# Performance work log

Measured on AMD Instinct MI355X. Metric: run time of the kernel, lower is better.

The kernel has to match this reference:

```python
import jax, jax.numpy as jnp
import numpy as np

H = 1024      # hidden_size
V = 50257     # output_size (vocab)
L = 512       # max_length (encoder steps)


def setup_inputs() -> dict:
    key = jax.random.key(0)
    ks = jax.random.split(key, 12)
    s = 0.02
    return {
        "input": jax.random.randint(ks[0], (1,), 0, V),
        "h": jax.random.normal(ks[1], (1, 1, H), dtype=jnp.float32),
        "c": jax.random.normal(ks[2], (1, 1, H), dtype=jnp.float32),
        "encoder_outputs": jax.random.normal(ks[3], (L, H), dtype=jnp.float32),
        "emb_table": jax.random.normal(ks[4], (V, H), dtype=jnp.float32) * s,
        "W_attn": jax.random.normal(ks[5], (L, 2 * H), dtype=jnp.float32) * s,
        "b_attn": jnp.zeros((L,), jnp.float32),
        "W_comb": jax.random.normal(ks[6], (H, 2 * H), dtype=jnp.float32) * s,
        "b_comb": jnp.zeros((H,), jnp.float32),
        "W_ih": jax.random.normal(ks[7], (4 * H, H), dtype=jnp.float32) * s,
        "W_hh": jax.random.normal(ks[8], (4 * H, H), dtype=jnp.float32) * s,
        "b_ih": jnp.zeros((4 * H,), jnp.float32),
        "b_hh": jnp.zeros((4 * H,), jnp.float32),
        "W_out": jax.random.normal(ks[9], (V, H), dtype=jnp.float32) * s,
        "b_out": jnp.zeros((V,), jnp.float32),
    }


def reference(input, h, c, encoder_outputs, emb_table, W_attn, b_attn,
              W_comb, b_comb, W_ih, W_hh, b_ih, b_hh, W_out, b_out):
    # Single decode step, batch=1. Dropout is identity (eval mode).
    embedded = emb_table[input]            # [1, H]
    h0 = h[0]                              # [1, H]
    c0 = c[0]                              # [1, H]

    # attention over encoder outputs
    attn_logits = jnp.concatenate([embedded, h0], axis=1) @ W_attn.T + b_attn  # [1, L]
    attn_weights = jax.nn.softmax(attn_logits, axis=1)                          # [1, L]
    attn_applied = attn_weights @ encoder_outputs                               # [1, H]

    # combine + relu
    x = jnp.concatenate([embedded, attn_applied], axis=1) @ W_comb.T + b_comb   # [1, H]
    x = jax.nn.relu(x)

    # single-step LSTM cell (PyTorch gate order: i, f, g, o)
    gates = x @ W_ih.T + b_ih + h0 @ W_hh.T + b_hh                              # [1, 4H]
    i_g, f_g, g_g, o_g = jnp.split(gates, 4, axis=1)
    c1 = jax.nn.sigmoid(f_g) * c0 + jax.nn.sigmoid(i_g) * jnp.tanh(g_g)
    h1 = jax.nn.sigmoid(o_g) * jnp.tanh(c1)

    # output projection + log-softmax
    logp = jax.nn.log_softmax(h1 @ W_out.T + b_out, axis=1)                     # [1, V]
    return (logp, h1[None], c1[None], attn_weights)
```

## Files before the change

### kernel.cpp

```cpp
#include <hip/hip_runtime.h>
#include <math.h>

#define H 1024
#define V 50257
#define L 512
#define RBLK 64

__device__ __forceinline__ float wave_sum(float v) {
#pragma unroll
    for (int off = 32; off; off >>= 1) v += __shfl_xor(v, off, 64);
    return v;
}
__device__ __forceinline__ float wave_max(float v) {
#pragma unroll
    for (int off = 32; off; off >>= 1) v = fmaxf(v, __shfl_xor(v, off, 64));
    return v;
}
__device__ __forceinline__ float sigmoidf(float x) { return 1.f / (1.f + expf(-x)); }

__global__ void k_attn_logits(const int* __restrict__ inp, const float* __restrict__ h0,
                              const float* __restrict__ emb_table,
                              const float* __restrict__ W_attn, const float* __restrict__ b_attn,
                              float* __restrict__ logits) {
    int wave = (blockIdx.x * blockDim.x + threadIdx.x) >> 6;
    int lane = threadIdx.x & 63;
    if (wave >= L) return;
    const float* emb = emb_table + (size_t)inp[0] * H;
    const float* wrow = W_attn + (size_t)wave * (2 * H);
    float acc = 0.f;
#pragma unroll
    for (int it = 0; it < 8; ++it) {
        int k = it * 256 + lane * 4;
        float4 wv = *(const float4*)(wrow + k);
        const float* src = (k < H) ? (emb + k) : (h0 + (k - H));
        float4 xv = *(const float4*)src;
        acc += wv.x * xv.x + wv.y * xv.y + wv.z * xv.z + wv.w * xv.w;
    }
    acc = wave_sum(acc);
    if (lane == 0) logits[wave] = acc + b_attn[wave];
}

__global__ void k_softmax(const float* __restrict__ logits, float* __restrict__ attn_w,
                          float* __restrict__ ws_aa) {
    __shared__ float sh[8];
    __shared__ float bc;
    int t = threadIdx.x, lane = t & 63, wid = t >> 6;
    float v = logits[t];
    float m = wave_max(v);
    if (lane == 0) sh[wid] = m;
    __syncthreads();
    if (t == 0) { float mm = sh[0]; for (int i = 1; i < 8; ++i) mm = fmaxf(mm, sh[i]); bc = mm; }
    __syncthreads();
    m = bc;
    float e = expf(v - m);
    float s = wave_sum(e);
    __syncthreads();
    if (lane == 0) sh[wid] = s;
    __syncthreads();
    if (t == 0) { float ss = 0.f; for (int i = 0; i < 8; ++i) ss += sh[i]; bc = ss; }
    __syncthreads();
    attn_w[t] = e / bc;
    ws_aa[t] = 0.f;
    ws_aa[t + 512] = 0.f;
}

__global__ void k_attn_applied(const float* __restrict__ attn_w, const float* __restrict__ enc,
                               float* __restrict__ ws_aa) {
    int b = blockIdx.x, t = threadIdx.x;
    float4 acc = make_float4(0.f, 0.f, 0.f, 0.f);
#pragma unroll
    for (int r = 0; r < 8; ++r) {
        int l = b * 8 + r;
        float w = attn_w[l];
        float4 e = *(const float4*)(enc + (size_t)l * H + t * 4);
        acc.x += w * e.x; acc.y += w * e.y; acc.z += w * e.z; acc.w += w * e.w;
    }
    atomicAdd(&ws_aa[t * 4 + 0], acc.x);
    atomicAdd(&ws_aa[t * 4 + 1], acc.y);
    atomicAdd(&ws_aa[t * 4 + 2], acc.z);
    atomicAdd(&ws_aa[t * 4 + 3], acc.w);
}

__global__ void k_comb(const int* __restrict__ inp, const float* __restrict__ emb_table,
                       const float* __restrict__ ws_aa, const float* __restrict__ W_comb,
                       const float* __restrict__ b_comb, float* __restrict__ ws_x) {
    int wave = (blockIdx.x * blockDim.x + threadIdx.x) >> 6;
    int lane = threadIdx.x & 63;
    if (wave >= H) return;
    const float* emb = emb_table + (size_t)inp[0] * H;
    const float* wrow = W_comb + (size_t)wave * (2 * H);
    float acc = 0.f;
#pragma unroll
    for (int it = 0; it < 8; ++it) {
        int k = it * 256 + lane * 4;
        float4 wv = *(const float4*)(wrow + k);
        const float* src = (k < H) ? (emb + k) : (ws_aa + (k - H));
        float4 xv = *(const float4*)src;
        acc += wv.x * xv.x + wv.y * xv.y + wv.z * xv.z + wv.w * xv.w;
    }
    acc = wave_sum(acc);
    if (lane == 0) ws_x[wave] = fmaxf(acc + b_comb[wave], 0.f);
}

__global__ void k_gates_lstm(const float* __restrict__ ws_x, const float* __restrict__ h0,
                             const float* __restrict__ c0,
                             const float* __restrict__ W_ih, const float* __restrict__ W_hh,
                             const float* __restrict__ b_ih, const float* __restrict__ b_hh,
                             float* __restrict__ out_h1, float* __restrict__ out_c1) {
    __shared__ float g[4];
    int j = blockIdx.x;
    int wv = threadIdx.x >> 6;
    int lane = threadIdx.x & 63;
    int row = wv * H + j;
    const float* wi = W_ih + (size_t)row * H;
    const float* wh = W_hh + (size_t)row * H;
    float acc = 0.f;
#pragma unroll
    for (int it = 0; it < 4; ++it) {
        int k = it * 256 + lane * 4;
        float4 a = *(const float4*)(wi + k);
        float4 xv = *(const float4*)(ws_x + k);
        acc += a.x * xv.x + a.y * xv.y + a.z * xv.z + a.w * xv.w;
        float4 b = *(const float4*)(wh + k);
        float4 hv = *(const float4*)(h0 + k);
        acc += b.x * hv.x + b.y * hv.y + b.z * hv.z + b.w * hv.w;
    }
    acc = wave_sum(acc);
    if (lane == 0) g[wv] = acc + b_ih[row] + b_hh[row];
    __syncthreads();
    if (threadIdx.x == 0) {
        float ig = sigmoidf(g[0]);
        float fg = sigmoidf(g[1]);
        float gg = tanhf(g[2]);
        float og = sigmoidf(g[3]);
        float c1 = fg * c0[j] + ig * gg;
        out_c1[j] = c1;
        out_h1[j] = og * tanhf(c1);
    }
}

__global__ void k_out(const float* __restrict__ h1, const float* __restrict__ W_out,
                      const float* __restrict__ b_out, float* __restrict__ logp) {
    int wave = (blockIdx.x * blockDim.x + threadIdx.x) >> 6;
    int lane = threadIdx.x & 63;
    if (wave >= V) return;
    const float* wrow = W_out + (size_t)wave * H;
    float acc = 0.f;
#pragma unroll
    for (int it = 0; it < 4; ++it) {
        int k = it * 256 + lane * 4;
        float4 wv = *(const float4*)(wrow + k);
        float4 hv = *(const float4*)(h1 + k);
        acc += wv.x * hv.x + wv.y * hv.y + wv.z * hv.z + wv.w * hv.w;
    }
    acc = wave_sum(acc);
    if (lane == 0) logp[wave] = acc + b_out[wave];
}

__global__ void k_red(const float* __restrict__ logp, float* __restrict__ pair) {
    __shared__ float sh[4];
    int t = threadIdx.x, lane = t & 63, wid = t >> 6;
    float vals[4];
    int n = 0;
    float m = -1e30f;
    for (int v = blockIdx.x * 256 + t; v < V; v += RBLK * 256) {
        vals[n] = logp[v];
        m = fmaxf(m, vals[n]);
        ++n;
    }
    m = wave_max(m);
    if (lane == 0) sh[wid] = m;
    __syncthreads();
    float m4 = fmaxf(fmaxf(sh[0], sh[1]), fmaxf(sh[2], sh[3]));
    float s = 0.f;
    for (int i = 0; i < n; ++i) s += expf(vals[i] - m4);
    s = wave_sum(s);
    __syncthreads();
    if (lane == 0) sh[wid] = s;
    __syncthreads();
    if (t == 0) {
        pair[blockIdx.x * 2]     = m4;
        pair[blockIdx.x * 2 + 1] = sh[0] + sh[1] + sh[2] + sh[3];
    }
}

__global__ void k_sub(float* __restrict__ logp, const float* __restrict__ pair) {
    float mg = -1e30f;
#pragma unroll
    for (int i = 0; i < RBLK; ++i) mg = fmaxf(mg, pair[2 * i]);
    float sg = 0.f;
#pragma unroll
    for (int i = 0; i < RBLK; ++i) sg += pair[2 * i + 1] * expf(pair[2 * i] - mg);
    float lse = mg + logf(sg);
    int v = blockIdx.x * blockDim.x + threadIdx.x;
    if (v < V) logp[v] -= lse;
}

extern "C" void kernel_launch(void* const* d_in, const int* in_sizes, int n_in,
                              void* d_out, int out_size, void* d_ws, size_t ws_size,
                              hipStream_t stream) {
    const int*   inp     = (const int*)d_in[0];
    const float* h0      = (const float*)d_in[1];
    const float* c0      = (const float*)d_in[2];
    const float* enc     = (const float*)d_in[3];
    const float* emb     = (const float*)d_in[4];
    const float* W_attn  = (const float*)d_in[5];
    const float* b_attn  = (const float*)d_in[6];
    const float* W_comb  = (const float*)d_in[7];
    const float* b_comb  = (const float*)d_in[8];
    const float* W_ih    = (const float*)d_in[9];
    const float* W_hh    = (const float*)d_in[10];
    const float* b_ih    = (const float*)d_in[11];
    const float* b_hh    = (const float*)d_in[12];
    const float* W_out   = (const float*)d_in[13];
    const float* b_out   = (const float*)d_in[14];

    float* out      = (float*)d_out;
    float* out_logp = out;
    float* out_h1   = out + V;
    float* out_c1   = out + V + H;
    float* out_attn = out + V + 2 * H;

    float* ws        = (float*)d_ws;
    float* ws_logits = ws;
    float* ws_aa     = ws + 512;
    float* ws_x      = ws + 512 + 1024;
    float* ws_pair   = ws + 512 + 2048;

    k_attn_logits<<<128, 256, 0, stream>>>(inp, h0, emb, W_attn, b_attn, ws_logits);
    k_softmax<<<1, 512, 0, stream>>>(ws_logits, out_attn, ws_aa);
    k_attn_applied<<<64, 256, 0, stream>>>(out_attn, enc, ws_aa);
    k_comb<<<256, 256, 0, stream>>>(inp, emb, ws_aa, W_comb, b_comb, ws_x);
    k_gates_lstm<<<1024, 256, 0, stream>>>(ws_x, h0, c0, W_ih, W_hh, b_ih, b_hh, out_h1, out_c1);
    k_out<<<(V + 3) / 4, 256, 0, stream>>>(out_h1, W_out, b_out, out_logp);
    k_red<<<RBLK, 256, 0, stream>>>(out_logp, ws_pair);
    k_sub<<<(V + 255) / 256, 256, 0, stream>>>(out_logp, ws_pair);
}
```

Baseline: 431.3 us.

## Fuse softmax into attention apply and online log-sum-exp into output projection

Merges the attention softmax with the attention-weighted sum so each of 64 blocks recomputes the softmax statistics itself, and moves the workspace zeroing into the logits kernel. The output projection becomes a persistent grid-stride kernel that keeps h1 in registers and maintains an online max and sum per block, which removes the separate reduction kernel and its re-read of the logits. The final subtract kernel merges 2048 partial pairs. This saves two launches and one pass over the vocab, at the cost of redundant softmax work per block and a fixed grid size for the largest matvec.

```diff
diff --git a/kernel.cpp b/kernel.cpp
--- a/kernel.cpp
+++ b/kernel.cpp
@@ -4,7 +4,8 @@
 #define H 1024
 #define V 50257
 #define L 512
-#define RBLK 64
+#define OUTB 2048
+#define OUTW (OUTB * 4)
 
 __device__ __forceinline__ float wave_sum(float v) {
 #pragma unroll
@@ -21,7 +22,8 @@
 __global__ void k_attn_logits(const int* __restrict__ inp, const float* __restrict__ h0,
                               const float* __restrict__ emb_table,
                               const float* __restrict__ W_attn, const float* __restrict__ b_attn,
-                              float* __restrict__ logits) {
+                              float* __restrict__ logits, float* __restrict__ ws_aa) {
+    if (blockIdx.x < 4) ws_aa[blockIdx.x * 256 + threadIdx.x] = 0.f;
     int wave = (blockIdx.x * blockDim.x + threadIdx.x) >> 6;
     int lane = threadIdx.x & 63;
     if (wave >= L) return;
@@ -40,38 +42,34 @@
     if (lane == 0) logits[wave] = acc + b_attn[wave];
 }
 
-__global__ void k_softmax(const float* __restrict__ logits, float* __restrict__ attn_w,
-                          float* __restrict__ ws_aa) {
-    __shared__ float sh[8];
-    __shared__ float bc;
+__global__ void k_softmax_attn(const float* __restrict__ logits, const float* __restrict__ enc,
+                               float* __restrict__ out_attn, float* __restrict__ ws_aa) {
+    __shared__ float sh[4];
+    __shared__ float shm, shs;
     int t = threadIdx.x, lane = t & 63, wid = t >> 6;
-    float v = logits[t];
-    float m = wave_max(v);
+    float v0 = logits[t], v1 = logits[t + 256];
+    float m = wave_max(fmaxf(v0, v1));
     if (lane == 0) sh[wid] = m;
     __syncthreads();
-    if (t == 0) { float mm = sh[0]; for (int i = 1; i < 8; ++i) mm = fmaxf(mm, sh[i]); bc = mm; }
-    __syncthreads();
-    m = bc;
-    float e = expf(v - m);
-    float s = wave_sum(e);
-    __syncthreads();
+    if (t == 0) shm = fmaxf(fmaxf(sh[0], sh[1]), fmaxf(sh[2], sh[3]));
+    __syncthreads();
+    m = shm;
+    float e0 = expf(v0 - m), e1 = expf(v1 - m);
+    float s = wave_sum(e0 + e1);
     if (lane == 0) sh[wid] = s;
     __syncthreads();
-    if (t == 0) { float ss = 0.f; for (int i = 0; i < 8; ++i) ss += sh[i]; bc = ss; }
-    __syncthreads();
-    attn_w[t] = e / bc;
-    ws_aa[t] = 0.f;
-    ws_aa[t + 512] = 0.f;
-}
-
-__global__ void k_attn_applied(const float* __restrict__ attn_w, const float* __restrict__ enc,
-                               float* __restrict__ ws_aa) {
-    int b = blockIdx.x, t = threadIdx.x;
+    if (t == 0) shs = sh[0] + sh[1] + sh[2] + sh[3];
+    __syncthreads();
+    float inv = 1.f / shs;
+    if (blockIdx.x == 0) {
+        out_attn[t]       = e0 * inv;
+        out_attn[t + 256] = e1 * inv;
+    }
     float4 acc = make_float4(0.f, 0.f, 0.f, 0.f);
 #pragma unroll
     for (int r = 0; r < 8; ++r) {
-        int l = b * 8 + r;
-        float w = attn_w[l];
+        int l = blockIdx.x * 8 + r;
+        float w = expf(logits[l] - m) * inv;
         float4 e = *(const float4*)(enc + (size_t)l * H + t * 4);
         acc.x += w * e.x; acc.y += w * e.y; acc.z += w * e.z; acc.w += w * e.w;
     }
@@ -140,59 +138,74 @@
 }
 
 __global__ void k_out(const float* __restrict__ h1, const float* __restrict__ W_out,
-                      const float* __restrict__ b_out, float* __restrict__ logp) {
-    int wave = (blockIdx.x * blockDim.x + threadIdx.x) >> 6;
-    int lane = threadIdx.x & 63;
-    if (wave >= V) return;
-    const float* wrow = W_out + (size_t)wave * H;
-    float acc = 0.f;
-#pragma unroll
-    for (int it = 0; it < 4; ++it) {
-        int k = it * 256 + lane * 4;
-        float4 wv = *(const float4*)(wrow + k);
-        float4 hv = *(const float4*)(h1 + k);
-        acc += wv.x * hv.x + wv.y * hv.y + wv.z * hv.z + wv.w * hv.w;
-    }
-    acc = wave_sum(acc);
-    if (lane == 0) logp[wave] = acc + b_out[wave];
-}
-
-__global__ void k_red(const float* __restrict__ logp, float* __restrict__ pair) {
-    __shared__ float sh[4];
-    int t = threadIdx.x, lane = t & 63, wid = t >> 6;
-    float vals[4];
-    int n = 0;
-    float m = -1e30f;
-    for (int v = blockIdx.x * 256 + t; v < V; v += RBLK * 256) {
-        vals[n] = logp[v];
-        m = fmaxf(m, vals[n]);
-        ++n;
-    }
-    m = wave_max(m);
-    if (lane == 0) sh[wid] = m;
-    __syncthreads();
-    float m4 = fmaxf(fmaxf(sh[0], sh[1]), fmaxf(sh[2], sh[3]));
-    float s = 0.f;
-    for (int i = 0; i < n; ++i) s += expf(vals[i] - m4);
-    s = wave_sum(s);
-    __syncthreads();
-    if (lane == 0) sh[wid] = s;
-    __syncthreads();
-    if (t == 0) {
-        pair[blockIdx.x * 2]     = m4;
-        pair[blockIdx.x * 2 + 1] = sh[0] + sh[1] + sh[2] + sh[3];
+                      const float* __restrict__ b_out, float* __restrict__ logp,
+                      float* __restrict__ pair) {
+    __shared__ float shm[4], shs[4];
+    int lane = threadIdx.x & 63, wv = threadIdx.x >> 6;
+    int w = blockIdx.x * 4 + wv;
+    float4 hv[4];
+#pragma unroll
+    for (int it = 0; it < 4; ++it) hv[it] = *(const float4*)(h1 + it * 256 + lane * 4);
+    float m = -INFINITY, s = 0.f;
+    for (int row = w; row < V; row += OUTW) {
+        const float* wrow = W_out + (size_t)row * H;
+        float acc = 0.f;
+#pragma unroll
+        for (int it = 0; it < 4; ++it) {
+            float4 a = *(const float4*)(wrow + it * 256 + lane * 4);
+            acc += a.x * hv[it].x + a.y * hv[it].y + a.z * hv[it].z + a.w * hv[it].w;
+        }
+        acc = wave_sum(acc) + b_out[row];
+        if (lane == 0) logp[row] = acc;
+        float nm = fmaxf(m, acc);
+        s = s * expf(m - nm) + expf(acc - nm);
+        m = nm;
+    }
+    if (lane == 0) { shm[wv] = m; shs[wv] = s; }
+    __syncthreads();
+    if (threadIdx.x == 0) {
+        float M = shm[0], S = shs[0];
+#pragma unroll
+        for (int i = 1; i < 4; ++i) {
+            float nm = fmaxf(M, shm[i]);
+            S = S * expf(M - nm) + shs[i] * expf(shm[i] - nm);
+            M = nm;
+        }
+        pair[blockIdx.x * 2]     = M;
+        pair[blockIdx.x * 2 + 1] = S;
     }
 }
 
 __global__ void k_sub(float* __restrict__ logp, const float* __restrict__ pair) {
-    float mg = -1e30f;
-#pragma unroll
-    for (int i = 0; i < RBLK; ++i) mg = fmaxf(mg, pair[2 * i]);
-    float sg = 0.f;
-#pragma unroll
-    for (int i = 0; i < RBLK; ++i) sg += pair[2 * i + 1] * expf(pair[2 * i] - mg);
-    float lse = mg + logf(sg);
-    int v = blockIdx.x * blockDim.x + threadIdx.x;
+    __shared__ float shm[4], shs[4];
+    int t = threadIdx.x, lane = t & 63, wv = t >> 6;
+    float m = -INFINITY, s = 0.f;
+#pragma unroll
+    for (int i = 0; i < 8; ++i) {
+        int p = i * 256 + t;
+        float pm = pair[p * 2], ps = pair[p * 2 + 1];
+        float nm = fmaxf(m, pm);
+        s = s * expf(m - nm) + ps * expf(pm - nm);
+        m = nm;
+    }
+#pragma unroll
+    for (int off = 32; off; off >>= 1) {
+        float om = __shfl_xor(m, off, 64), os = __shfl_xor(s, off, 64);
+        float nm = fmaxf(m, om);
+        s = s * expf(m - nm) + os * expf(om - nm);
+        m = nm;
+    }
+    if (lane == 0) { shm[wv] = m; shs[wv] = s; }
+    __syncthreads();
+    float M = shm[0], S = shs[0];
+#pragma unroll
+    for (int i = 1; i < 4; ++i) {
+        float nm = fmaxf(M, shm[i]);
+        S = S * expf(M - nm) + shs[i] * expf(shm[i] - nm);
+        M = nm;
+    }
+    float lse = M + logf(S);
+    int v = blockIdx.x * 256 + t;
     if (v < V) logp[v] -= lse;
 }
 
@@ -227,12 +240,10 @@
     float* ws_x      = ws + 512 + 1024;
     float* ws_pair   = ws + 512 + 2048;
 
-    k_attn_logits<<<128, 256, 0, stream>>>(inp, h0, emb, W_attn, b_attn, ws_logits);
-    k_softmax<<<1, 512, 0, stream>>>(ws_logits, out_attn, ws_aa);
-    k_attn_applied<<<64, 256, 0, stream>>>(out_attn, enc, ws_aa);
+    k_attn_logits<<<128, 256, 0, stream>>>(inp, h0, emb, W_attn, b_attn, ws_logits, ws_aa);
+    k_softmax_attn<<<64, 256, 0, stream>>>(ws_logits, enc, out_attn, ws_aa);
     k_comb<<<256, 256, 0, stream>>>(inp, emb, ws_aa, W_comb, b_comb, ws_x);
     k_gates_lstm<<<1024, 256, 0, stream>>>(ws_x, h0, c0, W_ih, W_hh, b_ih, b_hh, out_h1, out_c1);
-    k_out<<<(V + 3) / 4, 256, 0, stream>>>(out_h1, W_out, b_out, out_logp);
-    k_red<<<RBLK, 256, 0, stream>>>(out_logp, ws_pair);
+    k_out<<<OUTB, 256, 0, stream>>>(out_h1, W_out, b_out, out_logp, ws_pair);
     k_sub<<<(V + 255) / 256, 256, 0, stream>>>(out_logp, ws_pair);
 }
```

New measurement: 431.5 us. Within noise of the previous version (+0.0%).
